# Kernel tuning notes

Measured on AMD Instinct MI355X. Metric: run time of the kernel, lower is better.

## Reference

```python
import jax, jax.numpy as jnp
import numpy as np

N_NODES, N_EDGES, N_FEAT, N_GRAPHS = 100_000, 1_600_000, 3, 512
FENG = jnp.array([4, 8, 9, 12, 13, 14])  # feng_filters(): second-order pairs with scale2 > scale1
LEAKY_SLOPE = 0.01


def _wavelet_constructor():
    # Psi_j = P^{2^{j-1}} - P^{2^j}, j = 1..4, over 17 diffusion levels P^0..P^16
    W = np.zeros((4, 17), dtype=np.float32)
    for j, (a, b) in enumerate([(1, 2), (2, 4), (4, 8), (8, 16)]):
        W[j, a] = 1.0
        W[j, b] = -1.0
    return jnp.asarray(W)


def _gcn_edges(edge_index, n):
    # gcn_norm with self-loops: w_ij = d_i^-1/2 d_j^-1/2 on A + I
    loop = jnp.arange(n)
    src = jnp.concatenate([edge_index[0], loop])
    dst = jnp.concatenate([edge_index[1], loop])
    deg = jax.ops.segment_sum(jnp.ones_like(dst, dtype=jnp.float32), dst, num_segments=n)
    dinv = jnp.where(deg > 0, jax.lax.rsqrt(deg), 0.0)
    w = dinv[src] * dinv[dst]
    return src, dst, w


def _diffuse(x, src, dst, w, n):
    # lazy random walk: 0.5 * (x + P_norm x), x: [N, C, k]
    agg = jax.ops.segment_sum(w[:, None, None] * x[src], dst, num_segments=n)
    return 0.5 * (x + agg)


def _scatter_features(x, edge_index):
    n, c = x.shape
    src, dst, w = _gcn_edges(edge_index, n)
    Wav = _wavelet_constructor()

    s0 = x[:, :, None]                                   # [N, C, 1]
    levels = [s0]
    for _ in range(16):
        levels.append(_diffuse(levels[-1], src, dst, w, n))
    D = jnp.stack(levels)                                # [17, N, C, 1]
    sub = jnp.einsum('wt,tnck->wnck', Wav, D)[..., 0]    # [4, N, C]
    s1 = jnp.abs(jnp.transpose(sub, (1, 2, 0)))          # [N, C, 4]

    levels2 = [s1]
    for _ in range(16):
        levels2.append(_diffuse(levels2[-1], src, dst, w, n))
    D2 = jnp.stack(levels2)                              # [17, N, C, 4]
    sub2 = jnp.einsum('wt,tncf->wncf', Wav, D2)          # [4, N, C, 4]
    # reproduce the exact torch transpose/reshape sequence of LEGS Scatter
    t = jnp.abs(jnp.transpose(sub2, (1, 0, 2, 3)).reshape(n, c, 16))  # [N, C, 16]
    s2 = jnp.swapaxes(t, 1, 2)[:, FENG]                  # [N, 6, C]

    xcat = jnp.concatenate([s0, s1], axis=2)             # [N, C, 5]
    xcat = jnp.swapaxes(xcat, 1, 2)                      # [N, 5, C]
    xcat = jnp.concatenate([xcat, s2], axis=1)           # [N, 11, C]
    return xcat.reshape(n, 11 * c)                       # [N, 33]


def _scatter_moments(x, batch, num_graphs):
    # per-graph mean / variance / skew (3 central moments), concatenated -> [G, 3*F]
    cnt = jax.ops.segment_sum(jnp.ones((x.shape[0],), x.dtype), batch, num_segments=num_graphs)
    cnt = jnp.maximum(cnt, 1.0)[:, None]
    mean = jax.ops.segment_sum(x, batch, num_segments=num_graphs) / cnt
    dev = x - mean[batch]
    var = jax.ops.segment_sum(dev * dev, batch, num_segments=num_graphs) / cnt
    skew = jax.ops.segment_sum(dev * dev * dev, batch, num_segments=num_graphs) / cnt
    return jnp.concatenate([mean, var, skew], axis=1)


def setup_inputs() -> dict:
    key = jax.random.key(0)
    ks = jax.random.split(key, 8)
    x = jax.random.normal(ks[0], (N_NODES, N_FEAT), dtype=jnp.float32)
    edge_index = jax.random.randint(ks[1], (2, N_EDGES), 0, N_NODES)
    batch = jnp.sort(jax.random.randint(ks[2], (N_NODES,), 0, N_GRAPHS))

    def lin(k, fan_in, fan_out):
        k1, k2 = jax.random.split(k)
        bound = 1.0 / np.sqrt(fan_in)
        W = jax.random.uniform(k1, (fan_in, fan_out), minval=-bound, maxval=bound, dtype=jnp.float32)
        b = jax.random.uniform(k2, (fan_out,), minval=-bound, maxval=bound, dtype=jnp.float32)
        return W, b

    W1, b1 = lin(ks[3], 99, 128)
    W2, b2 = lin(ks[4], 128, 64)
    W3, b3 = lin(ks[5], 64, 64)
    We, be = lin(ks[6], 64, 32)
    Wc, bc = lin(ks[7], 32, 1)
    return {"x": x, "W1": W1, "b1": b1, "W2": W2, "b2": b2, "W3": W3, "b3": b3,
            "We": We, "be": be, "Wc": Wc, "bc": bc,
            "edge_index": edge_index, "batch": batch, "num_graphs": N_GRAPHS}


def reference(x, W1, b1, W2, b2, W3, b3, We, be, Wc, bc, edge_index, batch, num_graphs):
    act = lambda v: jax.nn.leaky_relu(v, LEAKY_SLOPE)
    feats = _scatter_features(x, edge_index)              # [N, 33]
    h = _scatter_moments(feats, batch, num_graphs)        # [G, 99]
    h = act(h)
    h = act(h @ W1 + b1)        # dropout is identity (p=0.0)
    h = act(h @ W2 + b2)
    h = h @ W3 + b3             # no activation before embedding layer (as in source)
    embedding = h @ We + be
    output = embedding @ Wc + bc  # classifier applied to embedding (pre-activation)
    return embedding, output
```

## Files before the change

### kernel.cpp

```cpp
#include <hip/hip_runtime.h>

#define N_NODES 100000
#define N_EDGES 1600000
#define NG      512
#define NPART   8
#define NPP     12500
#define CHUNK_E 8192

static __device__ __forceinline__ float lrelu(float v) {
    return v >= 0.0f ? v : 0.01f * v;
}

__global__ void k_zero_i32(int* __restrict__ p, int n) {
    int i = blockIdx.x * blockDim.x + threadIdx.x;
    if (i < n) p[i] = 0;
}

__global__ void k_copy_i32(const int* __restrict__ s, int* __restrict__ d, int n) {
    int i = blockIdx.x * blockDim.x + threadIdx.x;
    if (i < n) d[i] = s[i];
}

__global__ __launch_bounds__(256) void k_count_part(const int* __restrict__ edst,
                                                    int* __restrict__ counts) {
    int p = blockIdx.x & (NPART - 1);
    int chunk = blockIdx.x >> 3;
    int base = chunk * CHUNK_E;
    int plo = p * NPP, phi = plo + NPP;
    int end = base + CHUNK_E; if (end > N_EDGES) end = N_EDGES;
    for (int e = base + (int)threadIdx.x; e < end; e += 256) {
        int d = __builtin_nontemporal_load(&edst[e]);
        if (d >= plo && d < phi) atomicAdd(&counts[d], 1);
    }
}

__global__ void k_dinv(const int* __restrict__ counts, float* __restrict__ dinv,
                       float* __restrict__ dinv2, float* __restrict__ sdeg) {
    int i = blockIdx.x * blockDim.x + threadIdx.x;
    if (i < N_NODES) {
        float deg = (float)(counts[i] + 1);
        float s = sqrtf(deg);
        sdeg[i] = s;
        dinv[i] = 1.0f / s;
        dinv2[i] = 1.0f / deg;
    }
}

__global__ void k_scan_block(const int* __restrict__ counts, int* __restrict__ offsets,
                             int* __restrict__ bsums, int n) {
    __shared__ int tmp[1024];
    int gid = blockIdx.x * 1024 + threadIdx.x;
    int v = (gid < n) ? counts[gid] : 0;
    tmp[threadIdx.x] = v;
    __syncthreads();
    for (int off = 1; off < 1024; off <<= 1) {
        int t = (threadIdx.x >= off) ? tmp[threadIdx.x - off] : 0;
        __syncthreads();
        tmp[threadIdx.x] += t;
        __syncthreads();
    }
    if (gid < n) offsets[gid + 1] = tmp[threadIdx.x];
    if (threadIdx.x == 1023) bsums[blockIdx.x] = tmp[1023];
}

__global__ void k_scan_bsums(int* __restrict__ bsums, int nb) {
    if (blockIdx.x == 0 && threadIdx.x == 0) {
        int acc = 0;
        for (int b = 0; b < nb; ++b) { int v = bsums[b]; bsums[b] = acc; acc += v; }
    }
}

__global__ void k_scan_add(int* __restrict__ offsets, const int* __restrict__ bsums, int n) {
    int gid = blockIdx.x * 1024 + threadIdx.x;
    if (gid < n) offsets[gid + 1] += bsums[blockIdx.x];
    if (gid == 0) offsets[0] = 0;
}

__global__ __launch_bounds__(256) void k_scatter_part(
    const int* __restrict__ esrc, const int* __restrict__ edst,
    int* __restrict__ cursor, int* __restrict__ csr_src) {
    int p = blockIdx.x & (NPART - 1);
    int chunk = blockIdx.x >> 3;
    int base = chunk * CHUNK_E;
    int plo = p * NPP, phi = plo + NPP;
    int end = base + CHUNK_E; if (end > N_EDGES) end = N_EDGES;
    for (int e = base + (int)threadIdx.x; e < end; e += 256) {
        int d = __builtin_nontemporal_load(&edst[e]);
        if (d >= plo && d < phi) {
            int s = __builtin_nontemporal_load(&esrc[e]);
            int pos = atomicAdd(&cursor[d], 1);
            csr_src[pos] = s;
        }
    }
}

__global__ void k_vinit(const float* __restrict__ x, const float* __restrict__ dinv,
                        float4* __restrict__ v) {
    int i = blockIdx.x * blockDim.x + threadIdx.x;
    if (i >= N_NODES) return;
    float di = dinv[i];
    v[i] = make_float4(di * x[i * 3 + 0], di * x[i * 3 + 1], di * x[i * 3 + 2], 0.0f);
}

__global__ __launch_bounds__(256) void k_vdiff3(
    const float4* __restrict__ xin, float4* __restrict__ xout,
    const int* __restrict__ offs, const int* __restrict__ csrc,
    const float* __restrict__ dinv2) {
    int t = blockIdx.x * 256 + threadIdx.x;
    if (t >= N_NODES * 8) return;
    int h = t & 7;
    int i = t >> 3;
    int b = offs[i], e = offs[i + 1];
    float a0 = 0.0f, a1 = 0.0f, a2 = 0.0f;
    for (int p = b + h; p < e; p += 8) {
        int s = csrc[p];
        float4 xv = xin[s];
        a0 += xv.x; a1 += xv.y; a2 += xv.z;
    }
    a0 += __shfl_xor(a0, 1, 64); a1 += __shfl_xor(a1, 1, 64); a2 += __shfl_xor(a2, 1, 64);
    a0 += __shfl_xor(a0, 2, 64); a1 += __shfl_xor(a1, 2, 64); a2 += __shfl_xor(a2, 2, 64);
    a0 += __shfl_xor(a0, 4, 64); a1 += __shfl_xor(a1, 4, 64); a2 += __shfl_xor(a2, 4, 64);
    if (h == 0) {
        float d2 = dinv2[i];
        float4 sv = xin[i];
        xout[i] = make_float4(0.5f * (sv.x + d2 * (a0 + sv.x)),
                              0.5f * (sv.y + d2 * (a1 + sv.y)),
                              0.5f * (sv.z + d2 * (a2 + sv.z)), 0.0f);
    }
}

__global__ __launch_bounds__(256) void k_vdiff12(
    const float4* __restrict__ xin, float4* __restrict__ xout,
    const int* __restrict__ offs, const int* __restrict__ csrc,
    const float* __restrict__ dinv2) {
    int t = blockIdx.x * 256 + threadIdx.x;
    if (t >= N_NODES * 8) return;
    int h = t & 7;
    int i = t >> 3;
    int b = offs[i], e = offs[i + 1];
    float a[12];
#pragma unroll
    for (int c = 0; c < 12; ++c) a[c] = 0.0f;
    for (int p = b + h; p < e; p += 8) {
        int s = csrc[p];
        float4 b0 = xin[s * 3 + 0];
        float4 b1 = xin[s * 3 + 1];
        float4 b2 = xin[s * 3 + 2];
        a[0] += b0.x; a[1] += b0.y; a[2]  += b0.z; a[3]  += b0.w;
        a[4] += b1.x; a[5] += b1.y; a[6]  += b1.z; a[7]  += b1.w;
        a[8] += b2.x; a[9] += b2.y; a[10] += b2.z; a[11] += b2.w;
    }
#pragma unroll
    for (int c = 0; c < 12; ++c) {
        a[c] += __shfl_xor(a[c], 1, 64);
        a[c] += __shfl_xor(a[c], 2, 64);
        a[c] += __shfl_xor(a[c], 4, 64);
    }
    if (h == 0) {
        float d2 = dinv2[i];
        float4 s0 = xin[i * 3 + 0], s1 = xin[i * 3 + 1], s2 = xin[i * 3 + 2];
        xout[i * 3 + 0] = make_float4(0.5f * (s0.x + d2 * (a[0] + s0.x)),
                                      0.5f * (s0.y + d2 * (a[1] + s0.y)),
                                      0.5f * (s0.z + d2 * (a[2] + s0.z)),
                                      0.5f * (s0.w + d2 * (a[3] + s0.w)));
        xout[i * 3 + 1] = make_float4(0.5f * (s1.x + d2 * (a[4] + s1.x)),
                                      0.5f * (s1.y + d2 * (a[5] + s1.y)),
                                      0.5f * (s1.z + d2 * (a[6] + s1.z)),
                                      0.5f * (s1.w + d2 * (a[7] + s1.w)));
        xout[i * 3 + 2] = make_float4(0.5f * (s2.x + d2 * (a[8] + s2.x)),
                                      0.5f * (s2.y + d2 * (a[9] + s2.y)),
                                      0.5f * (s2.z + d2 * (a[10] + s2.z)),
                                      0.5f * (s2.w + d2 * (a[11] + s2.w)));
    }
}

__global__ void k_s1v(const float4* __restrict__ L1, const float4* __restrict__ L2,
                      const float4* __restrict__ L4, const float4* __restrict__ L8,
                      const float4* __restrict__ L16, float* __restrict__ s1v) {
    int i = blockIdx.x * blockDim.x + threadIdx.x;
    if (i >= N_NODES) return;
    float4 v[5];
    v[0] = L1[i]; v[1] = L2[i]; v[2] = L4[i]; v[3] = L8[i]; v[4] = L16[i];
    float* out = s1v + (size_t)i * 12;
#pragma unroll
    for (int f = 0; f < 4; ++f) {
        out[0 * 4 + f] = fabsf(v[f].x - v[f + 1].x);
        out[1 * 4 + f] = fabsf(v[f].y - v[f + 1].y);
        out[2 * 4 + f] = fabsf(v[f].z - v[f + 1].z);
    }
}

__global__ void k_feats(const float* __restrict__ x, const float* __restrict__ s1v,
                        const float* __restrict__ M1, const float* __restrict__ M2,
                        const float* __restrict__ M4, const float* __restrict__ M8,
                        const float* __restrict__ M16, const float* __restrict__ sdeg,
                        float* __restrict__ feats) {
    int i = blockIdx.x * blockDim.x + threadIdx.x;
    if (i >= N_NODES) return;
    float sd = sdeg[i];
    float* out = feats + (size_t)i * 33;
    out[0] = x[i * 3 + 0];
    out[1] = x[i * 3 + 1];
    out[2] = x[i * 3 + 2];
    for (int r = 1; r <= 4; ++r)
        for (int c = 0; c < 3; ++c)
            out[r * 3 + c] = sd * s1v[(size_t)i * 12 + c * 4 + (r - 1)];
    const float* Ms[5] = {M1, M2, M4, M8, M16};
    const int FENG[6] = {4, 8, 9, 12, 13, 14};
    for (int m = 0; m < 6; ++m) {
        for (int c2 = 0; c2 < 3; ++c2) {
            int idx = c2 * 16 + FENG[m];
            int w = idx / 12, rem = idx % 12, cc = rem / 4, f = rem % 4;
            float v = Ms[w][(size_t)i * 12 + cc * 4 + f] - Ms[w + 1][(size_t)i * 12 + cc * 4 + f];
            out[(5 + m) * 3 + c2] = fabsf(sd * v);
        }
    }
}

static __device__ __forceinline__ int lower_bound_i(const int* __restrict__ a, int n, int key) {
    int lo = 0, hi = n;
    while (lo < hi) { int mid = (lo + hi) >> 1; if (a[mid] < key) lo = mid + 1; else hi = mid; }
    return lo;
}

__global__ __launch_bounds__(256) void k_moments_mean(
    const float* __restrict__ feats, const int* __restrict__ batch,
    float* __restrict__ meanbuf) {
    __shared__ float part[4][33];
    int g = blockIdx.x;
    int lo = lower_bound_i(batch, N_NODES, g);
    int hi = lower_bound_i(batch, N_NODES, g + 1);
    float acc[33];
#pragma unroll
    for (int c = 0; c < 33; ++c) acc[c] = 0.0f;
    for (int i = lo + (int)threadIdx.x; i < hi; i += 256) {
        const float* f = feats + (size_t)i * 33;
#pragma unroll
        for (int c = 0; c < 33; ++c) acc[c] += f[c];
    }
#pragma unroll
    for (int c = 0; c < 33; ++c) {
        float v = acc[c];
        for (int o = 32; o >= 1; o >>= 1) v += __shfl_down(v, o, 64);
        acc[c] = v;
    }
    int wid = threadIdx.x >> 6, lane = threadIdx.x & 63;
    if (lane == 0)
        for (int c = 0; c < 33; ++c) part[wid][c] = acc[c];
    __syncthreads();
    if (threadIdx.x < 33) {
        float cnt = (float)((hi - lo) > 1 ? (hi - lo) : 1);
        float s = part[0][threadIdx.x] + part[1][threadIdx.x] +
                  part[2][threadIdx.x] + part[3][threadIdx.x];
        meanbuf[g * 33 + threadIdx.x] = s / cnt;
    }
}

__global__ __launch_bounds__(256) void k_moments_vs(
    const float* __restrict__ feats, const int* __restrict__ batch,
    const float* __restrict__ meanbuf, float* __restrict__ h0) {
    __shared__ float part2[4][33];
    __shared__ float part3[4][33];
    int g = blockIdx.x;
    int lo = lower_bound_i(batch, N_NODES, g);
    int hi = lower_bound_i(batch, N_NODES, g + 1);
    float mu[33], a2[33], a3[33];
#pragma unroll
    for (int c = 0; c < 33; ++c) { mu[c] = meanbuf[g * 33 + c]; a2[c] = 0.0f; a3[c] = 0.0f; }
    for (int i = lo + (int)threadIdx.x; i < hi; i += 256) {
        const float* f = feats + (size_t)i * 33;
#pragma unroll
        for (int c = 0; c < 33; ++c) {
            float d = f[c] - mu[c];
            float d2 = d * d;
            a2[c] += d2;
            a3[c] += d2 * d;
        }
    }
#pragma unroll
    for (int c = 0; c < 33; ++c) {
        float v2 = a2[c], v3 = a3[c];
        for (int o = 32; o >= 1; o >>= 1) {
            v2 += __shfl_down(v2, o, 64);
            v3 += __shfl_down(v3, o, 64);
        }
        a2[c] = v2; a3[c] = v3;
    }
    int wid = threadIdx.x >> 6, lane = threadIdx.x & 63;
    if (lane == 0)
        for (int c = 0; c < 33; ++c) { part2[wid][c] = a2[c]; part3[wid][c] = a3[c]; }
    __syncthreads();
    if (threadIdx.x < 33) {
        int c = threadIdx.x;
        float cnt = (float)((hi - lo) > 1 ? (hi - lo) : 1);
        float v2 = part2[0][c] + part2[1][c] + part2[2][c] + part2[3][c];
        float v3 = part3[0][c] + part3[1][c] + part3[2][c] + part3[3][c];
        h0[g * 99 + c]      = lrelu(mu[c]);
        h0[g * 99 + 33 + c] = lrelu(v2 / cnt);
        h0[g * 99 + 66 + c] = lrelu(v3 / cnt);
    }
}

__global__ __launch_bounds__(128) void k_mlp(
    const float* __restrict__ h0,
    const float* __restrict__ W1, const float* __restrict__ b1,
    const float* __restrict__ W2, const float* __restrict__ b2,
    const float* __restrict__ W3, const float* __restrict__ b3,
    const float* __restrict__ We, const float* __restrict__ be,
    const float* __restrict__ Wc, const float* __restrict__ bc,
    float* __restrict__ emb, float* __restrict__ outp) {
    __shared__ float s0[99], s1[128], s2[64], s3[64], s4[32];
    int g = blockIdx.x;
    int t = threadIdx.x;
    if (t < 99) s0[t] = h0[g * 99 + t];
    __syncthreads();
    {
        float a = b1[t];
        for (int k = 0; k < 99; ++k) a += s0[k] * W1[k * 128 + t];
        s1[t] = lrelu(a);
    }
    __syncthreads();
    if (t < 64) {
        float a = b2[t];
        for (int k = 0; k < 128; ++k) a += s1[k] * W2[k * 64 + t];
        s2[t] = lrelu(a);
    }
    __syncthreads();
    if (t < 64) {
        float a = b3[t];
        for (int k = 0; k < 64; ++k) a += s2[k] * W3[k * 64 + t];
        s3[t] = a;
    }
    __syncthreads();
    if (t < 32) {
        float a = be[t];
        for (int k = 0; k < 64; ++k) a += s3[k] * We[k * 32 + t];
        s4[t] = a;
        emb[g * 32 + t] = a;
    }
    __syncthreads();
    if (t == 0) {
        float a = bc[0];
        for (int k = 0; k < 32; ++k) a += s4[k] * Wc[k];
        outp[g] = a;
    }
}

extern "C" void kernel_launch(void* const* d_in, const int* in_sizes, int n_in,
                              void* d_out, int out_size, void* d_ws, size_t ws_size,
                              hipStream_t stream) {
    const float* x   = (const float*)d_in[0];
    const float* W1  = (const float*)d_in[1];
    const float* b1  = (const float*)d_in[2];
    const float* W2  = (const float*)d_in[3];
    const float* b2  = (const float*)d_in[4];
    const float* W3  = (const float*)d_in[5];
    const float* b3  = (const float*)d_in[6];
    const float* We  = (const float*)d_in[7];
    const float* be  = (const float*)d_in[8];
    const float* Wc  = (const float*)d_in[9];
    const float* bc  = (const float*)d_in[10];
    const int*   eix = (const int*)d_in[11];
    const int*   batch = (const int*)d_in[12];
    const int* esrc = eix;
    const int* edst = eix + N_EDGES;

    char* ws = (char*)d_ws;
    size_t off = 0;
    auto alloc = [&](size_t bytes) -> void* {
        void* p = ws + off;
        off = (off + bytes + 255) & ~(size_t)255;
        return p;
    };
    int*   counts  = (int*)alloc((size_t)N_NODES * 4);
    int*   offsets = (int*)alloc((size_t)(N_NODES + 1) * 4);
    int*   cursor  = (int*)alloc((size_t)N_NODES * 4);
    float* dinv    = (float*)alloc((size_t)N_NODES * 4);
    float* dinv2   = (float*)alloc((size_t)N_NODES * 4);
    float* sdeg    = (float*)alloc((size_t)N_NODES * 4);
    int*   bsums   = (int*)alloc(1024 * 4);
    int*   csr_src = (int*)alloc((size_t)N_EDGES * 4);
    float4* v0     = (float4*)alloc((size_t)N_NODES * 16);
    float4* p1[7];
    for (int i = 0; i < 7; ++i) p1[i] = (float4*)alloc((size_t)N_NODES * 16);
    float* s1v = (float*)alloc((size_t)N_NODES * 12 * 4);
    float* p2[7];
    for (int i = 0; i < 7; ++i) p2[i] = (float*)alloc((size_t)N_NODES * 12 * 4);
    float* feats = (float*)alloc((size_t)N_NODES * 33 * 4);
    float* meanb = (float*)alloc((size_t)NG * 33 * 4);
    float* h0 = (float*)alloc((size_t)NG * 99 * 4);
    (void)ws_size; (void)in_sizes; (void)n_in; (void)out_size;

    const int TB = 256;
    const int gbN = (N_NODES + TB - 1) / TB;
    const int nbScan = (N_NODES + 1023) / 1024;
    const int nChunks = (N_EDGES + CHUNK_E - 1) / CHUNK_E;
    const int gbPart = nChunks * NPART;

    hipLaunchKernelGGL(k_zero_i32, dim3(gbN), dim3(TB), 0, stream, counts, N_NODES);
    hipLaunchKernelGGL(k_count_part, dim3(gbPart), dim3(TB), 0, stream, edst, counts);
    hipLaunchKernelGGL(k_dinv, dim3(gbN), dim3(TB), 0, stream, counts, dinv, dinv2, sdeg);
    hipLaunchKernelGGL(k_scan_block, dim3(nbScan), dim3(1024), 0, stream, counts, offsets, bsums, N_NODES);
    hipLaunchKernelGGL(k_scan_bsums, dim3(1), dim3(1), 0, stream, bsums, nbScan);
    hipLaunchKernelGGL(k_scan_add, dim3(nbScan), dim3(1024), 0, stream, offsets, bsums, N_NODES);
    hipLaunchKernelGGL(k_copy_i32, dim3(gbN), dim3(TB), 0, stream, offsets, cursor, N_NODES);
    hipLaunchKernelGGL(k_scatter_part, dim3(gbPart), dim3(TB), 0, stream, esrc, edst, cursor, csr_src);

    hipLaunchKernelGGL(k_vinit, dim3(gbN), dim3(TB), 0, stream, x, dinv, v0);

    const int saveT[5] = {1, 2, 4, 8, 16};

    const float4* prev = v0;
    float4* saves1[5];
    {
        int si = 0, sc = 0;
        const int gb = (N_NODES * 8 + TB - 1) / TB;
        for (int t = 1; t <= 16; ++t) {
            float4* outb;
            if (si < 5 && t == saveT[si]) { outb = p1[si]; saves1[si] = outb; ++si; }
            else { outb = p1[5 + sc]; sc ^= 1; }
            hipLaunchKernelGGL(k_vdiff3, dim3(gb), dim3(TB), 0, stream,
                               prev, outb, offsets, csr_src, dinv2);
            prev = outb;
        }
    }
    hipLaunchKernelGGL(k_s1v, dim3(gbN), dim3(TB), 0, stream,
                       saves1[0], saves1[1], saves1[2], saves1[3], saves1[4], s1v);

    float* saves2[5];
    {
        const float* prev2 = s1v;
        int si = 0, sc = 0;
        const int gb = (N_NODES * 8 + TB - 1) / TB;
        for (int t = 1; t <= 16; ++t) {
            float* outb;
            if (si < 5 && t == saveT[si]) { outb = p2[si]; saves2[si] = outb; ++si; }
            else { outb = p2[5 + sc]; sc ^= 1; }
            hipLaunchKernelGGL(k_vdiff12, dim3(gb), dim3(TB), 0, stream,
                               (const float4*)prev2, (float4*)outb, offsets, csr_src, dinv2);
            prev2 = outb;
        }
    }

    hipLaunchKernelGGL(k_feats, dim3(gbN), dim3(TB), 0, stream,
                       x, s1v, saves2[0], saves2[1], saves2[2], saves2[3], saves2[4], sdeg, feats);
    hipLaunchKernelGGL(k_moments_mean, dim3(NG), dim3(256), 0, stream, feats, batch, meanb);
    hipLaunchKernelGGL(k_moments_vs, dim3(NG), dim3(256), 0, stream, feats, batch, meanb, h0);

    float* emb  = (float*)d_out;
    float* outp = (float*)d_out + NG * 32;
    hipLaunchKernelGGL(k_mlp, dim3(NG), dim3(128), 0, stream,
                       h0, W1, b1, W2, b2, W3, b3, We, be, Wc, bc, emb, outp);
}
```

Baseline: 832.5 us.

## Bin edges by destination partition before CSR build; split vdiff12 by float4 quarter

Replaces the eight-way repeated scans of the edge list in count and scatter with one binning pass. That pass buckets (src,dst) pairs into per-partition global buffers through shared-memory queues. Counting then uses shared-memory histograms per partition, and the scatter reads only its own partition's bucket. Separately, the 12-channel diffusion kernel now assigns 12 threads per node, each handling one float4 slot over a quarter of the edges, instead of 8 threads each gathering all three float4s. This trades register pressure and extra edge re-reads for more parallelism. The binning adds a large intermediate buffer with a fixed capacity and more synchronisation.

```diff
diff --git a/kernel.cpp b/kernel.cpp
--- a/kernel.cpp
+++ b/kernel.cpp
@@ -5,7 +5,11 @@
 #define NG      512
 #define NPART   8
 #define NPP     12500
-#define CHUNK_E 8192
+#define BCAP    245760
+#define BQ      1024
+#define BFLUSH  512
+#define NBBLK   256
+#define EPB     ((N_EDGES + NBBLK - 1) / NBBLK)
 
 static __device__ __forceinline__ float lrelu(float v) {
     return v >= 0.0f ? v : 0.01f * v;
@@ -19,19 +23,6 @@
 __global__ void k_copy_i32(const int* __restrict__ s, int* __restrict__ d, int n) {
     int i = blockIdx.x * blockDim.x + threadIdx.x;
     if (i < n) d[i] = s[i];
-}
-
-__global__ __launch_bounds__(256) void k_count_part(const int* __restrict__ edst,
-                                                    int* __restrict__ counts) {
-    int p = blockIdx.x & (NPART - 1);
-    int chunk = blockIdx.x >> 3;
-    int base = chunk * CHUNK_E;
-    int plo = p * NPP, phi = plo + NPP;
-    int end = base + CHUNK_E; if (end > N_EDGES) end = N_EDGES;
-    for (int e = base + (int)threadIdx.x; e < end; e += 256) {
-        int d = __builtin_nontemporal_load(&edst[e]);
-        if (d >= plo && d < phi) atomicAdd(&counts[d], 1);
-    }
 }
 
 __global__ void k_dinv(const int* __restrict__ counts, float* __restrict__ dinv,
@@ -46,6 +37,86 @@
     }
 }
 
+__global__ __launch_bounds__(256) void k_bin(const int* __restrict__ esrc,
+                                             const int* __restrict__ edst,
+                                             int* __restrict__ gcur,
+                                             uint2* __restrict__ gbuf) {
+    __shared__ uint2 buf[NPART][BQ];
+    __shared__ int lcnt[NPART];
+    __shared__ int gbase[NPART];
+    if (threadIdx.x < NPART) lcnt[threadIdx.x] = 0;
+    __syncthreads();
+    int base = blockIdx.x * EPB;
+    int end = base + EPB; if (end > N_EDGES) end = N_EDGES;
+    for (int r = base; r < end; r += 2048) {
+        int rend = r + 2048; if (rend > end) rend = end;
+        for (int e = r + (int)threadIdx.x; e < rend; e += 256) {
+            int d = edst[e];
+            int s = esrc[e];
+            int b = d / NPP;
+            int pos = atomicAdd(&lcnt[b], 1);
+            if (pos < BQ) {
+                buf[b][pos] = make_uint2((unsigned)s, (unsigned)d);
+            } else {
+                int g = atomicAdd(&gcur[b], 1);
+                gbuf[(size_t)b * BCAP + g] = make_uint2((unsigned)s, (unsigned)d);
+            }
+        }
+        __syncthreads();
+        for (int b = 0; b < NPART; ++b) {
+            int cnt = lcnt[b];
+            if (cnt >= BFLUSH) {
+                if (threadIdx.x == 0) gbase[b] = atomicAdd(&gcur[b], BFLUSH);
+                __syncthreads();
+                int gb = gbase[b];
+                for (int i = threadIdx.x; i < BFLUSH; i += 256)
+                    gbuf[(size_t)b * BCAP + gb + i] = buf[b][i];
+                __syncthreads();
+                int inb = cnt < BQ ? cnt : BQ;
+                int rem = inb - BFLUSH;
+                for (int i = threadIdx.x; i < rem; i += 256)
+                    buf[b][i] = buf[b][BFLUSH + i];
+                __syncthreads();
+                if (threadIdx.x == 0) lcnt[b] = rem;
+                __syncthreads();
+            }
+        }
+    }
+    for (int b = 0; b < NPART; ++b) {
+        int cnt = lcnt[b]; if (cnt > BQ) cnt = BQ;
+        if (cnt > 0) {
+            if (threadIdx.x == 0) gbase[b] = atomicAdd(&gcur[b], cnt);
+            __syncthreads();
+            int gb = gbase[b];
+            for (int i = threadIdx.x; i < cnt; i += 256)
+                gbuf[(size_t)b * BCAP + gb + i] = buf[b][i];
+        }
+        __syncthreads();
+    }
+}
+
+__global__ __launch_bounds__(1024) void k_count_b(const int* __restrict__ gcur,
+                                                  const uint2* __restrict__ gbuf,
+                                                  int* __restrict__ counts) {
+    __shared__ int h[NPP];
+    int p = blockIdx.x & (NPART - 1);
+    int slice = blockIdx.x >> 3;
+    for (int i = threadIdx.x; i < NPP; i += 1024) h[i] = 0;
+    __syncthreads();
+    int n = gcur[p];
+    int per = (n + 7) / 8;
+    int lo = slice * per, hi = lo + per; if (hi > n) hi = n;
+    const uint2* bb = gbuf + (size_t)p * BCAP;
+    int pl = p * NPP;
+    for (int i = lo + (int)threadIdx.x; i < hi; i += 1024) {
+        int d = (int)bb[i].y - pl;
+        atomicAdd(&h[d], 1);
+    }
+    __syncthreads();
+    for (int i = threadIdx.x; i < NPP; i += 1024)
+        if (h[i]) atomicAdd(&counts[pl + i], h[i]);
+}
+
 __global__ void k_scan_block(const int* __restrict__ counts, int* __restrict__ offsets,
                              int* __restrict__ bsums, int n) {
     __shared__ int tmp[1024];
@@ -76,21 +147,20 @@
     if (gid == 0) offsets[0] = 0;
 }
 
-__global__ __launch_bounds__(256) void k_scatter_part(
-    const int* __restrict__ esrc, const int* __restrict__ edst,
-    int* __restrict__ cursor, int* __restrict__ csr_src) {
+__global__ __launch_bounds__(256) void k_scatter_b(const int* __restrict__ gcur,
+                                                   const uint2* __restrict__ gbuf,
+                                                   int* __restrict__ cursor,
+                                                   int* __restrict__ csr_src) {
     int p = blockIdx.x & (NPART - 1);
-    int chunk = blockIdx.x >> 3;
-    int base = chunk * CHUNK_E;
-    int plo = p * NPP, phi = plo + NPP;
-    int end = base + CHUNK_E; if (end > N_EDGES) end = N_EDGES;
-    for (int e = base + (int)threadIdx.x; e < end; e += 256) {
-        int d = __builtin_nontemporal_load(&edst[e]);
-        if (d >= plo && d < phi) {
-            int s = __builtin_nontemporal_load(&esrc[e]);
-            int pos = atomicAdd(&cursor[d], 1);
-            csr_src[pos] = s;
-        }
+    int slice = blockIdx.x >> 3;
+    int n = gcur[p];
+    int per = (n + 15) / 16;
+    int lo = slice * per, hi = lo + per; if (hi > n) hi = n;
+    const uint2* bb = gbuf + (size_t)p * BCAP;
+    for (int i = lo + (int)threadIdx.x; i < hi; i += 256) {
+        uint2 e = bb[i];
+        int pos = atomicAdd(&cursor[e.y], 1);
+        csr_src[pos] = (int)e.x;
     }
 }
 
@@ -134,43 +204,29 @@
     const int* __restrict__ offs, const int* __restrict__ csrc,
     const float* __restrict__ dinv2) {
     int t = blockIdx.x * 256 + threadIdx.x;
-    if (t >= N_NODES * 8) return;
-    int h = t & 7;
-    int i = t >> 3;
+    if (t >= N_NODES * 12) return;
+    int i = t / 12;
+    int r = t % 12;
+    int q = r >> 2;
+    int h = r & 3;
     int b = offs[i], e = offs[i + 1];
-    float a[12];
-#pragma unroll
-    for (int c = 0; c < 12; ++c) a[c] = 0.0f;
-    for (int p = b + h; p < e; p += 8) {
+    float ax = 0.0f, ay = 0.0f, az = 0.0f, aw = 0.0f;
+    for (int p = b + h; p < e; p += 4) {
         int s = csrc[p];
-        float4 b0 = xin[s * 3 + 0];
-        float4 b1 = xin[s * 3 + 1];
-        float4 b2 = xin[s * 3 + 2];
-        a[0] += b0.x; a[1] += b0.y; a[2]  += b0.z; a[3]  += b0.w;
-        a[4] += b1.x; a[5] += b1.y; a[6]  += b1.z; a[7]  += b1.w;
-        a[8] += b2.x; a[9] += b2.y; a[10] += b2.z; a[11] += b2.w;
-    }
-#pragma unroll
-    for (int c = 0; c < 12; ++c) {
-        a[c] += __shfl_xor(a[c], 1, 64);
-        a[c] += __shfl_xor(a[c], 2, 64);
-        a[c] += __shfl_xor(a[c], 4, 64);
-    }
+        float4 xv = xin[s * 3 + q];
+        ax += xv.x; ay += xv.y; az += xv.z; aw += xv.w;
+    }
+    ax += __shfl_xor(ax, 1, 64); ay += __shfl_xor(ay, 1, 64);
+    az += __shfl_xor(az, 1, 64); aw += __shfl_xor(aw, 1, 64);
+    ax += __shfl_xor(ax, 2, 64); ay += __shfl_xor(ay, 2, 64);
+    az += __shfl_xor(az, 2, 64); aw += __shfl_xor(aw, 2, 64);
     if (h == 0) {
         float d2 = dinv2[i];
-        float4 s0 = xin[i * 3 + 0], s1 = xin[i * 3 + 1], s2 = xin[i * 3 + 2];
-        xout[i * 3 + 0] = make_float4(0.5f * (s0.x + d2 * (a[0] + s0.x)),
-                                      0.5f * (s0.y + d2 * (a[1] + s0.y)),
-                                      0.5f * (s0.z + d2 * (a[2] + s0.z)),
-                                      0.5f * (s0.w + d2 * (a[3] + s0.w)));
-        xout[i * 3 + 1] = make_float4(0.5f * (s1.x + d2 * (a[4] + s1.x)),
-                                      0.5f * (s1.y + d2 * (a[5] + s1.y)),
-                                      0.5f * (s1.z + d2 * (a[6] + s1.z)),
-                                      0.5f * (s1.w + d2 * (a[7] + s1.w)));
-        xout[i * 3 + 2] = make_float4(0.5f * (s2.x + d2 * (a[8] + s2.x)),
-                                      0.5f * (s2.y + d2 * (a[9] + s2.y)),
-                                      0.5f * (s2.z + d2 * (a[10] + s2.z)),
-                                      0.5f * (s2.w + d2 * (a[11] + s2.w)));
+        float4 sv = xin[i * 3 + q];
+        xout[i * 3 + q] = make_float4(0.5f * (sv.x + d2 * (ax + sv.x)),
+                                      0.5f * (sv.y + d2 * (ay + sv.y)),
+                                      0.5f * (sv.z + d2 * (az + sv.z)),
+                                      0.5f * (sv.w + d2 * (aw + sv.w)));
     }
 }
 
@@ -379,6 +435,8 @@
     float* dinv2   = (float*)alloc((size_t)N_NODES * 4);
     float* sdeg    = (float*)alloc((size_t)N_NODES * 4);
     int*   bsums   = (int*)alloc(1024 * 4);
+    int*   gcur    = (int*)alloc(NPART * 4);
+    uint2* gbuf    = (uint2*)alloc((size_t)NPART * BCAP * 8);
     int*   csr_src = (int*)alloc((size_t)N_EDGES * 4);
     float4* v0     = (float4*)alloc((size_t)N_NODES * 16);
     float4* p1[7];
@@ -394,17 +452,17 @@
     const int TB = 256;
     const int gbN = (N_NODES + TB - 1) / TB;
     const int nbScan = (N_NODES + 1023) / 1024;
-    const int nChunks = (N_EDGES + CHUNK_E - 1) / CHUNK_E;
-    const int gbPart = nChunks * NPART;
 
     hipLaunchKernelGGL(k_zero_i32, dim3(gbN), dim3(TB), 0, stream, counts, N_NODES);
-    hipLaunchKernelGGL(k_count_part, dim3(gbPart), dim3(TB), 0, stream, edst, counts);
+    hipLaunchKernelGGL(k_zero_i32, dim3(1), dim3(TB), 0, stream, gcur, NPART);
+    hipLaunchKernelGGL(k_bin, dim3(NBBLK), dim3(TB), 0, stream, esrc, edst, gcur, gbuf);
+    hipLaunchKernelGGL(k_count_b, dim3(64), dim3(1024), 0, stream, gcur, gbuf, counts);
     hipLaunchKernelGGL(k_dinv, dim3(gbN), dim3(TB), 0, stream, counts, dinv, dinv2, sdeg);
     hipLaunchKernelGGL(k_scan_block, dim3(nbScan), dim3(1024), 0, stream, counts, offsets, bsums, N_NODES);
     hipLaunchKernelGGL(k_scan_bsums, dim3(1), dim3(1), 0, stream, bsums, nbScan);
     hipLaunchKernelGGL(k_scan_add, dim3(nbScan), dim3(1024), 0, stream, offsets, bsums, N_NODES);
     hipLaunchKernelGGL(k_copy_i32, dim3(gbN), dim3(TB), 0, stream, offsets, cursor, N_NODES);
-    hipLaunchKernelGGL(k_scatter_part, dim3(gbPart), dim3(TB), 0, stream, esrc, edst, cursor, csr_src);
+    hipLaunchKernelGGL(k_scatter_b, dim3(128), dim3(TB), 0, stream, gcur, gbuf, cursor, csr_src);
 
     hipLaunchKernelGGL(k_vinit, dim3(gbN), dim3(TB), 0, stream, x, dinv, v0);
 
@@ -431,7 +489,7 @@
     {
         const float* prev2 = s1v;
         int si = 0, sc = 0;
-        const int gb = (N_NODES * 8 + TB - 1) / TB;
+        const int gb = (N_NODES * 12 + TB - 1) / TB;
         for (int t = 1; t <= 16; ++t) {
             float* outb;
             if (si < 5 && t == saveT[si]) { outb = p2[si]; saves2[si] = outb; ++si; }
```

After: 847.2 us. About the same (+1.8%).
